# Kernel optimization log

Measured on AMD Instinct MI355X. Metric: run time of the kernel, lower is better.

Reference implementation:

```python
import jax, jax.numpy as jnp
import numpy as np

EMBED = 1024
HEADS = 16


def setup_inputs() -> dict:
    key = jax.random.key(0)
    k1, k2, k3 = jax.random.split(key, 3)
    B, S, D = 2, 2048, EMBED
    x = jax.random.normal(k1, (B, S, D), dtype=jnp.float32)
    # nn.Linear weights: stored as [out, in]; y = x @ W.T
    w_qkv = jax.random.normal(k2, (3 * D, D), dtype=jnp.float32) * (D ** -0.5)
    w_out = jax.random.normal(k3, (D, D), dtype=jnp.float32) * (D ** -0.5)
    return {"x": x, "w_qkv": w_qkv, "w_out": w_out}


def reference(x, w_qkv, w_out):
    B, S, D = x.shape
    H = HEADS
    hd = D // H
    qkv = x @ w_qkv.T                       # [B, S, 3D]
    q, k, v = jnp.split(qkv, 3, axis=-1)
    # 'b l (head k) -> b head l k'
    def heads(t):
        return t.reshape(B, S, H, hd).transpose(0, 2, 1, 3)
    q, k, v = heads(q), heads(k), heads(v)
    scale = hd ** 0.5
    scores = jnp.einsum('bhqd,bhkd->bhqk', q, k) / scale
    probs = jax.nn.softmax(scores, axis=-1)
    out = jnp.einsum('bhqk,bhkd->bhqd', probs, v)  # [B, H, S, hd]
    out = out.transpose(0, 2, 1, 3).reshape(B, S, D)
    return out @ w_out.T
```

## Files before the change

kernel.cpp:

```cpp
#include <hip/hip_runtime.h>

typedef short short8 __attribute__((ext_vector_type(8)));
typedef short short4v __attribute__((ext_vector_type(4)));
typedef float floatx4 __attribute__((ext_vector_type(4)));
typedef unsigned short ushort_t;

#define EMBED 1024
#define HEADS 16
#define HD 64
#define SEQ 2048
#define BATCH 2
#define QSCALE 0.18033688f

__device__ inline ushort_t f2bf(float f) {
    unsigned int u = __float_as_uint(f);
    u += 0x7fff + ((u >> 16) & 1);
    return (ushort_t)(u >> 16);
}

typedef const __attribute__((address_space(1))) unsigned int* gas_t;
typedef __attribute__((address_space(3))) unsigned int* las_t;
__device__ inline void async_copy16(const ushort_t* g, ushort_t* l) {
    __builtin_amdgcn_global_load_lds((gas_t)g, (las_t)l, 16, 0, 0);
}

__global__ void cast3_kernel(const float* __restrict__ a, ushort_t* __restrict__ oa, int na,
                             const float* __restrict__ b, ushort_t* __restrict__ ob, int nb,
                             const float* __restrict__ c, ushort_t* __restrict__ oc, int nc) {
    int idx = (blockIdx.x * blockDim.x + threadIdx.x) * 4;
    const float* in; ushort_t* out;
    if (idx < na)            { in = a;  out = oa; }
    else if (idx < na + nb)  { in = b;  out = ob; idx -= na; }
    else if (idx < na + nb + nc) { in = c; out = oc; idx -= na + nb; }
    else return;
    float4 f = *(const float4*)(in + idx);
    ushort4 o;
    o.x = f2bf(f.x); o.y = f2bf(f.y); o.z = f2bf(f.z); o.w = f2bf(f.w);
    *(ushort4*)(out + idx) = o;
}

#define BM 128
#define BK 64

template<int MODE, int TBN>
__launch_bounds__(256, 3)
__global__ void gemm_bt(const ushort_t* __restrict__ A, const ushort_t* __restrict__ B,
                        float* __restrict__ outF,
                        ushort_t* __restrict__ qb, ushort_t* __restrict__ kb,
                        ushort_t* __restrict__ vtb,
                        int M, int N, int K) {
    __shared__ ushort_t As[BM * BK];
    __shared__ ushort_t Bs[TBN * BK];
    const int id   = blockIdx.x;
    const int jj   = id >> 3;
    const int bm   = (id & 7) * 4 + (jj & 3);
    const int bn   = jj >> 2;
    const int t    = threadIdx.x;
    const int lane = t & 63;
    const int wave = t >> 6;
    const int wm   = (wave >> 1) * 64;
    const int wn   = (wave & 1) * (TBN / 2);
    const int m0   = bm * BM;
    const int n0   = bn * TBN;
    const int col  = lane & 15;
    const int quad = lane >> 4;
    constexpr int NJ = TBN / 32;

    const int srow = lane >> 3;
    const int sgr  = (lane & 7) ^ (srow & 7);
    const int slot0 = quad ^ (col & 7);

    floatx4 acc[4][NJ] = {};

    for (int k0 = 0; k0 < K; k0 += BK) {
        for (int half = 0; half < 4; ++half) {
            int row0 = wave * 32 + half * 8;
            int r = row0 + srow;
            async_copy16(A + (size_t)(m0 + r) * K + k0 + sgr * 8, &As[row0 * BK]);
        }
        for (int half = 0; half < TBN / 32; ++half) {
            int row0 = wave * (TBN / 4) + half * 8;
            int r = row0 + srow;
            async_copy16(B + (size_t)(n0 + r) * K + k0 + sgr * 8, &Bs[row0 * BK]);
        }
        __syncthreads();
        short8 a[2][4], b[2][NJ];
        for (int i = 0; i < 4; ++i) {
            int base = (wm + i * 16 + col) * BK;
            a[0][i] = *(const short8*)(&As[base + slot0 * 8]);
            a[1][i] = *(const short8*)(&As[base + (slot0 ^ 4) * 8]);
        }
        for (int j = 0; j < NJ; ++j) {
            int base = (wn + j * 16 + col) * BK;
            b[0][j] = *(const short8*)(&Bs[base + slot0 * 8]);
            b[1][j] = *(const short8*)(&Bs[base + (slot0 ^ 4) * 8]);
        }
        for (int kk = 0; kk < 2; ++kk)
            for (int i = 0; i < 4; ++i)
                for (int j = 0; j < NJ; ++j)
                    acc[i][j] = __builtin_amdgcn_mfma_f32_16x16x32_bf16(a[kk][i], b[kk][j], acc[i][j], 0, 0, 0);
        __syncthreads();
    }

    for (int i = 0; i < 4; ++i)
        for (int j = 0; j < NJ; ++j) {
            int n = n0 + wn + j * 16 + col;
            int mb = m0 + wm + i * 16 + quad * 4;
            if (MODE == 1) {
                for (int r = 0; r < 4; ++r)
                    outF[(size_t)(mb + r) * N + n] = acc[i][j][r];
            } else {
                int part = n >> 10;
                int within = n & 1023;
                int h = within >> 6, d = within & 63;
                int bb = mb >> 11, s = mb & 2047;
                if (part == 2) {
                    short4v pv;
                    pv.x = (short)f2bf(acc[i][j][0]); pv.y = (short)f2bf(acc[i][j][1]);
                    pv.z = (short)f2bf(acc[i][j][2]); pv.w = (short)f2bf(acc[i][j][3]);
                    *(short4v*)(vtb + (((size_t)bb * HEADS + h) * HD + d) * SEQ + s) = pv;
                } else {
                    ushort_t* dst = (part == 0) ? qb : kb;
                    const float scl = (part == 0) ? QSCALE : 1.0f;
                    for (int r = 0; r < 4; ++r)
                        dst[(((size_t)bb * HEADS + h) * SEQ + s + r) * HD + d] = f2bf(acc[i][j][r] * scl);
                }
            }
        }
}

__launch_bounds__(512, 4)
__global__ void attn_kernel(const ushort_t* __restrict__ qb_, const ushort_t* __restrict__ kb,
                            const ushort_t* __restrict__ vtb, ushort_t* __restrict__ attn) {
    __shared__ __align__(16) ushort_t lds[32768];
    const int id   = blockIdx.x;
    const int jj   = id >> 3;
    const int bh   = (id & 7) * 4 + (jj >> 4);
    const int qblk = jj & 15;
    const int t    = threadIdx.x;
    const int lane = t & 63;
    const int wave = t >> 6;
    const int g    = wave >> 2;
    const int wv   = wave & 3;
    const int col  = lane & 15;
    const int quad = lane >> 4;
    const int q0   = qblk * 128 + wv * 32;
    const int sw   = col & 7;
    const int srow = lane >> 3;
    const int sgr  = lane & 7;

    const ushort_t* Q  = qb_ + (size_t)bh * SEQ * HD;
    const ushort_t* Kp = kb  + (size_t)bh * SEQ * HD;
    const ushort_t* Vt = vtb + (size_t)bh * HD * SEQ;

    ushort_t* Kb0 = &lds[g * 8192];
    ushort_t* Vb0 = &lds[16384 + g * 8192];

    auto stage = [&](int c, int buf) {
        int kt = c << 6;
        #pragma unroll
        for (int inst = 0; inst < 2; ++inst) {
            int row0 = wv * 16 + inst * 8;
            int r = row0 + srow;
            async_copy16(Kp + (size_t)(kt + r) * HD + (sgr ^ (r & 7)) * 8,
                         Kb0 + buf * 4096 + row0 * 64);
            async_copy16(Vt + (size_t)r * SEQ + kt + (sgr ^ (r & 7)) * 8,
                         Vb0 + buf * 4096 + row0 * 64);
        }
    };

    short8 qf[2][2];
    #pragma unroll
    for (int qt = 0; qt < 2; ++qt) {
        qf[qt][0] = *(const short8*)(Q + (size_t)(q0 + qt * 16 + col) * HD + quad * 8);
        qf[qt][1] = *(const short8*)(Q + (size_t)(q0 + qt * 16 + col) * HD + 32 + quad * 8);
    }

    const short4v onesf = { (short)0x3F80, (short)0x3F80, (short)0x3F80, (short)0x3F80 };

    floatx4 acc[2][4] = {};
    floatx4 accl[2] = {};

    stage(g, 0);
    __syncthreads();

    for (int i = 0; i < 16; ++i) {
        const int cur = i & 1;
        if (i < 15) stage(2 * (i + 1) + g, cur ^ 1);
        const ushort_t* Kc = Kb0 + cur * 4096;
        const ushort_t* Vc = Vb0 + cur * 4096;

        #pragma unroll
        for (int h = 0; h < 2; ++h) {
            short8 kf[2][2];
            short4v vf[4][2];
            #pragma unroll
            for (int nl = 0; nl < 2; ++nl) {
                int row = (2 * h + nl) * 16 + col;
                kf[nl][0] = *(const short8*)(Kc + row * 64 + ((quad ^ sw) * 8));
                kf[nl][1] = *(const short8*)(Kc + row * 64 + (((4 + quad) ^ sw) * 8));
            }
            #pragma unroll
            for (int dt = 0; dt < 4; ++dt)
                #pragma unroll
                for (int kl = 0; kl < 2; ++kl) {
                    int ks = h * 2 + kl;
                    int row = dt * 16 + col;
                    int slot = (ks * 2 + (quad >> 1)) ^ sw;
                    vf[dt][kl] = *(const short4v*)(Vc + row * 64 + slot * 8 + (quad & 1) * 4);
                }
            #pragma unroll
            for (int qt = 0; qt < 2; ++qt)
                #pragma unroll
                for (int nl = 0; nl < 2; ++nl) {
                    floatx4 z = {};
                    __builtin_amdgcn_s_setprio(1);
                    z = __builtin_amdgcn_mfma_f32_16x16x32_bf16(kf[nl][0], qf[qt][0], z, 0, 0, 0);
                    z = __builtin_amdgcn_mfma_f32_16x16x32_bf16(kf[nl][1], qf[qt][1], z, 0, 0, 0);
                    __builtin_amdgcn_s_setprio(0);
                    unsigned u0 = __float_as_uint(__builtin_amdgcn_exp2f(z[0]));
                    unsigned u1 = __float_as_uint(__builtin_amdgcn_exp2f(z[1]));
                    unsigned u2 = __float_as_uint(__builtin_amdgcn_exp2f(z[2]));
                    unsigned u3 = __float_as_uint(__builtin_amdgcn_exp2f(z[3]));
                    uint2 pk;
                    pk.x = __builtin_amdgcn_perm(u1, u0, 0x07060302u);
                    pk.y = __builtin_amdgcn_perm(u3, u2, 0x07060302u);
                    short4v pb = *(short4v*)&pk;
                    __builtin_amdgcn_s_setprio(1);
                    accl[qt] = __builtin_amdgcn_mfma_f32_16x16x16bf16_1k(
                        onesf, pb, accl[qt], 0, 0, 0);
                    #pragma unroll
                    for (int dt = 0; dt < 4; ++dt)
                        acc[qt][dt] = __builtin_amdgcn_mfma_f32_16x16x16bf16_1k(
                            vf[dt][nl], pb, acc[qt][dt], 0, 0, 0);
                    __builtin_amdgcn_s_setprio(0);
                }
        }
        __syncthreads();
    }

    float lsum[2] = { accl[0][0], accl[1][0] };

    float* fs = (float*)lds;
    const int slot = (wave * 64 + lane) * 20;
    floatx4 accK[4];
    float lsK;
    if (g == 0) {
        #pragma unroll
        for (int d = 0; d < 4; ++d) { *(floatx4*)(&fs[slot + d * 4]) = acc[1][d]; accK[d] = acc[0][d]; }
        fs[slot + 16] = lsum[1]; lsK = lsum[0];
    } else {
        #pragma unroll
        for (int d = 0; d < 4; ++d) { *(floatx4*)(&fs[slot + d * 4]) = acc[0][d]; accK[d] = acc[1][d]; }
        fs[slot + 16] = lsum[0]; lsK = lsum[1];
    }
    __syncthreads();
    const int pslot = ((wave ^ 4) * 64 + lane) * 20;
    #pragma unroll
    for (int d = 0; d < 4; ++d)
        accK[d] += *(const floatx4*)(&fs[pslot + d * 4]);
    float s = lsK + fs[pslot + 16];
    float inv = 1.0f / s;

    int b = bh >> 4, hh = bh & 15;
    int row = q0 + g * 16 + col;
    #pragma unroll
    for (int dt = 0; dt < 4; ++dt) {
        short4v o;
        o.x = (short)f2bf(accK[dt][0] * inv);
        o.y = (short)f2bf(accK[dt][1] * inv);
        o.z = (short)f2bf(accK[dt][2] * inv);
        o.w = (short)f2bf(accK[dt][3] * inv);
        *(short4v*)(attn + ((size_t)b * SEQ + row) * EMBED + hh * HD + dt * 16 + quad * 4) = o;
    }
}

extern "C" void kernel_launch(void* const* d_in, const int* in_sizes, int n_in,
                              void* d_out, int out_size, void* d_ws, size_t ws_size,
                              hipStream_t stream) {
    const float* x     = (const float*)d_in[0];
    const float* w_qkv = (const float*)d_in[1];
    const float* w_out = (const float*)d_in[2];
    float* out = (float*)d_out;

    char* ws = (char*)d_ws;
    size_t off = 0;
    ushort_t* x_bf    = (ushort_t*)(ws + off); off += (size_t)BATCH * SEQ * EMBED * 2;
    ushort_t* wqkv_bf = (ushort_t*)(ws + off); off += (size_t)3 * EMBED * EMBED * 2;
    ushort_t* wout_bf = (ushort_t*)(ws + off); off += (size_t)EMBED * EMBED * 2;
    ushort_t* q_buf   = (ushort_t*)(ws + off); off += (size_t)BATCH * HEADS * SEQ * HD * 2;
    ushort_t* k_buf   = (ushort_t*)(ws + off); off += (size_t)BATCH * HEADS * SEQ * HD * 2;
    ushort_t* vt_buf  = (ushort_t*)(ws + off); off += (size_t)BATCH * HEADS * SEQ * HD * 2;
    ushort_t* attn_bf = (ushort_t*)(ws + off); off += (size_t)BATCH * SEQ * EMBED * 2;

    int n_x = BATCH * SEQ * EMBED, n_wq = 3 * EMBED * EMBED, n_wo = EMBED * EMBED;
    int n_all = n_x + n_wq + n_wo;
    cast3_kernel<<<n_all / 1024, 256, 0, stream>>>(x, x_bf, n_x, w_qkv, wqkv_bf, n_wq,
                                                   w_out, wout_bf, n_wo);

    gemm_bt<0, 128><<<768, 256, 0, stream>>>(
        x_bf, wqkv_bf, nullptr, q_buf, k_buf, vt_buf, BATCH * SEQ, 3 * EMBED, EMBED);

    attn_kernel<<<512, 512, 0, stream>>>(q_buf, k_buf, vt_buf, attn_bf);

    gemm_bt<1, 64><<<512, 256, 0, stream>>>(
        attn_bf, wout_bf, out, nullptr, nullptr, nullptr, BATCH * SEQ, EMBED, EMBED);
}
```

Before: 170.7 us.

## Use 16x16x32 MFMA for PV and row-sum with permuted K rows

Replaces the pairs of 16x16x16 bf16 MFMAs in the P·V and row-sum accumulation with single 16x16x32 MFMAs. K rows are loaded in a permuted order so that two score tiles pack into one 8-element B operand, and V fragments become single 16-byte LDS reads. It also introduces a new XOR swizzle function for the LDS layout of K and V to keep bank conflicts low under the new access pattern. This halves the PV MFMA instruction count and V LDS reads, at the cost of holding more exp results live before issue.

```diff
diff --git a/kernel.cpp b/kernel.cpp
--- a/kernel.cpp
+++ b/kernel.cpp
@@ -145,9 +145,10 @@
     const int col  = lane & 15;
     const int quad = lane >> 4;
     const int q0   = qblk * 128 + wv * 32;
-    const int sw   = col & 7;
     const int srow = lane >> 3;
     const int sgr  = lane & 7;
+
+    auto swz = [](int r) { return (r & 7) ^ ((r >> 1) & 4) ^ ((r >> 3) & 2); };
 
     const ushort_t* Q  = qb_ + (size_t)bh * SEQ * HD;
     const ushort_t* Kp = kb  + (size_t)bh * SEQ * HD;
@@ -162,9 +163,10 @@
         for (int inst = 0; inst < 2; ++inst) {
             int row0 = wv * 16 + inst * 8;
             int r = row0 + srow;
-            async_copy16(Kp + (size_t)(kt + r) * HD + (sgr ^ (r & 7)) * 8,
+            int gr = sgr ^ swz(r);
+            async_copy16(Kp + (size_t)(kt + r) * HD + gr * 8,
                          Kb0 + buf * 4096 + row0 * 64);
-            async_copy16(Vt + (size_t)r * SEQ + kt + (sgr ^ (r & 7)) * 8,
+            async_copy16(Vt + (size_t)r * SEQ + kt + gr * 8,
                          Vb0 + buf * 4096 + row0 * 64);
         }
     };
@@ -176,7 +178,8 @@
         qf[qt][1] = *(const short8*)(Q + (size_t)(q0 + qt * 16 + col) * HD + 32 + quad * 8);
     }
 
-    const short4v onesf = { (short)0x3F80, (short)0x3F80, (short)0x3F80, (short)0x3F80 };
+    const short8 ones8 = { (short)0x3F80, (short)0x3F80, (short)0x3F80, (short)0x3F80,
+                           (short)0x3F80, (short)0x3F80, (short)0x3F80, (short)0x3F80 };
 
     floatx4 acc[2][4] = {};
     floatx4 accl[2] = {};
@@ -192,25 +195,22 @@
 
         #pragma unroll
         for (int h = 0; h < 2; ++h) {
-            short8 kf[2][2];
-            short4v vf[4][2];
+            short8 kf[2][2], vf8[4];
             #pragma unroll
             for (int nl = 0; nl < 2; ++nl) {
-                int row = (2 * h + nl) * 16 + col;
-                kf[nl][0] = *(const short8*)(Kc + row * 64 + ((quad ^ sw) * 8));
-                kf[nl][1] = *(const short8*)(Kc + row * 64 + (((4 + quad) ^ sw) * 8));
+                int krow = h * 32 + ((col >> 2) << 3) + (col & 3) + nl * 4;
+                int sk = swz(krow);
+                kf[nl][0] = *(const short8*)(Kc + krow * 64 + ((quad ^ sk) * 8));
+                kf[nl][1] = *(const short8*)(Kc + krow * 64 + (((4 + quad) ^ sk) * 8));
             }
             #pragma unroll
-            for (int dt = 0; dt < 4; ++dt)
-                #pragma unroll
-                for (int kl = 0; kl < 2; ++kl) {
-                    int ks = h * 2 + kl;
-                    int row = dt * 16 + col;
-                    int slot = (ks * 2 + (quad >> 1)) ^ sw;
-                    vf[dt][kl] = *(const short4v*)(Vc + row * 64 + slot * 8 + (quad & 1) * 4);
-                }
+            for (int dt = 0; dt < 4; ++dt) {
+                int vrow = dt * 16 + col;
+                vf8[dt] = *(const short8*)(Vc + vrow * 64 + (((h * 4 + quad) ^ swz(vrow)) * 8));
+            }
             #pragma unroll
-            for (int qt = 0; qt < 2; ++qt)
+            for (int qt = 0; qt < 2; ++qt) {
+                unsigned pk[4];
                 #pragma unroll
                 for (int nl = 0; nl < 2; ++nl) {
                     floatx4 z = {};
@@ -222,19 +222,19 @@
                     unsigned u1 = __float_as_uint(__builtin_amdgcn_exp2f(z[1]));
                     unsigned u2 = __float_as_uint(__builtin_amdgcn_exp2f(z[2]));
                     unsigned u3 = __float_as_uint(__builtin_amdgcn_exp2f(z[3]));
-                    uint2 pk;
-                    pk.x = __builtin_amdgcn_perm(u1, u0, 0x07060302u);
-                    pk.y = __builtin_amdgcn_perm(u3, u2, 0x07060302u);
-                    short4v pb = *(short4v*)&pk;
-                    __builtin_amdgcn_s_setprio(1);
-                    accl[qt] = __builtin_amdgcn_mfma_f32_16x16x16bf16_1k(
-                        onesf, pb, accl[qt], 0, 0, 0);
-                    #pragma unroll
-                    for (int dt = 0; dt < 4; ++dt)
-                        acc[qt][dt] = __builtin_amdgcn_mfma_f32_16x16x16bf16_1k(
-                            vf[dt][nl], pb, acc[qt][dt], 0, 0, 0);
-                    __builtin_amdgcn_s_setprio(0);
+                    pk[nl * 2 + 0] = __builtin_amdgcn_perm(u1, u0, 0x07060302u);
+                    pk[nl * 2 + 1] = __builtin_amdgcn_perm(u3, u2, 0x07060302u);
                 }
+                short8 pb8 = *(short8*)pk;
+                __builtin_amdgcn_s_setprio(1);
+                accl[qt] = __builtin_amdgcn_mfma_f32_16x16x32_bf16(
+                    ones8, pb8, accl[qt], 0, 0, 0);
+                #pragma unroll
+                for (int dt = 0; dt < 4; ++dt)
+                    acc[qt][dt] = __builtin_amdgcn_mfma_f32_16x16x32_bf16(
+                        vf8[dt], pb8, acc[qt][dt], 0, 0, 0);
+                __builtin_amdgcn_s_setprio(0);
+            }
         }
         __syncthreads();
     }
```

Result: faster. 162.2 us (median of 2 runs) (-5.0%).
